# Kernel optimization log

Hardware: AMD Instinct MI355X
Metric: run time of the kernel (lower is better)

## Reference

```python
import jax, jax.numpy as jnp
import numpy as np

C = 64            # in_channels
IC = C // 2       # inter_channels (channel_rate=2)
R = 16            # reduction_ratio
EPS = 1e-5


def setup_inputs() -> dict:
    key = jax.random.key(0)
    ks = jax.random.split(key, 16)
    s = 0.05
    return {
        "x": jax.random.normal(ks[0], (16, C, 64, 25), dtype=jnp.float32),
        # 1x1 conv projections (common_v, key, query): [out, in] + bias
        "Wv": jax.random.normal(ks[1], (IC, C), dtype=jnp.float32) * s,
        "bv": jax.random.normal(ks[2], (IC,), dtype=jnp.float32) * s,
        "Wk": jax.random.normal(ks[3], (IC, C), dtype=jnp.float32) * s,
        "bk": jax.random.normal(ks[4], (IC,), dtype=jnp.float32) * s,
        "Wq": jax.random.normal(ks[5], (IC, C), dtype=jnp.float32) * s,
        "bq": jax.random.normal(ks[6], (IC,), dtype=jnp.float32) * s,
        # Trans_s: conv1x1 back to C + BatchNorm2d params (nonzero so output is non-trivial)
        "Wt": jax.random.normal(ks[7], (C, IC), dtype=jnp.float32) * s,
        "bt": jax.random.normal(ks[8], (C,), dtype=jnp.float32) * s,
        "gamma": jax.random.normal(ks[9], (C,), dtype=jnp.float32) * 0.5 + 1.0,
        "beta": jax.random.normal(ks[10], (C,), dtype=jnp.float32) * s,
        # ChannelGate MLP: Linear(C, C//R), Linear(C//R, C)
        "W1": jax.random.normal(ks[11], (C // R, C), dtype=jnp.float32) * s,
        "b1": jax.random.normal(ks[12], (C // R,), dtype=jnp.float32) * s,
        "W2": jax.random.normal(ks[13], (C, C // R), dtype=jnp.float32) * s,
        "b2": jax.random.normal(ks[14], (C,), dtype=jnp.float32) * s,
    }


def _conv1x1(x, W, b):
    # x: [N, Cin, T, V]; W: [Cout, Cin]
    return jnp.einsum('nctv,oc->notv', x, W) + b[None, :, None, None]


def reference(x, Wv, bv, Wk, bk, Wq, bq, Wt, bt, gamma, beta, W1, b1, W2, b2):
    N, Cc, T, V = x.shape
    TV = T * V
    ic = Wv.shape[0]

    v_x = _conv1x1(x, Wv, bv).reshape(N, ic, TV).transpose(0, 2, 1)  # [N, TV, ic]
    k_x = _conv1x1(x, Wk, bk).reshape(N, ic, TV).transpose(0, 2, 1)  # [N, TV, ic]
    q_x = _conv1x1(x, Wq, bq).reshape(N, ic, TV)                      # [N, ic, TV]

    # Unscaled dot-product attention over TV tokens (full [N, TV, TV] matrix)
    A = jnp.einsum('nti,nis->nts', k_x, q_x)
    attn = jax.nn.softmax(A, axis=-1)
    p = jnp.einsum('nts,nsi->nti', attn, v_x)                         # [N, TV, ic]
    p = p.transpose(0, 2, 1).reshape(N, ic, T, V)

    # Trans_s: conv1x1 + BatchNorm2d (training-mode batch statistics)
    p = _conv1x1(p, Wt, bt)
    mean = p.mean(axis=(0, 2, 3), keepdims=True)
    var = p.var(axis=(0, 2, 3), keepdims=True)
    p = (p - mean) * jax.lax.rsqrt(var + EPS)
    p = p * gamma[None, :, None, None] + beta[None, :, None, None]

    # ChannelGate (avg pool only) applied to original x
    avg = x.mean(axis=(2, 3))                                          # [N, C]
    h = jax.nn.relu(avg @ W1.T + b1)
    gate = jax.nn.sigmoid(h @ W2.T + b2)                               # [N, C]

    return gate[:, :, None, None] * p + x
```

## Files before the change

kernel.cpp:

```cpp
#include <hip/hip_runtime.h>
#include <hip/hip_bf16.h>
#include <math.h>

#define NB   16
#define CC   64
#define ICH  32
#define TV   1600
#define NTV  (NB*TV)

typedef __bf16 bf16x8 __attribute__((ext_vector_type(8)));
typedef __bf16 bf16x4 __attribute__((ext_vector_type(4)));
typedef float  f32x4  __attribute__((ext_vector_type(4)));

__global__ __launch_bounds__(256) void proj_gate_kernel(
    const float* __restrict__ x,
    const float* __restrict__ Wv, const float* __restrict__ bv,
    const float* __restrict__ Wk, const float* __restrict__ bk,
    const float* __restrict__ Wq, const float* __restrict__ bq,
    __bf16* __restrict__ Qb, __bf16* __restrict__ Kb,
    __bf16* __restrict__ VTb, float* __restrict__ AVG) {
  if (blockIdx.x >= 1248) {
    int b = blockIdx.x - 1248;
    int n = b >> 2, cq = b & 3;
    int c16 = threadIdx.x >> 4, l = threadIdx.x & 15;
    int c = cq * 16 + c16;
    const float4* xp = (const float4*)(x + ((size_t)n * CC + c) * TV) + l;
    float s = 0.f;
#pragma unroll
    for (int i = 0; i < 25; ++i) {
      float4 v = xp[i * 16];
      s += v.x + v.y + v.z + v.w;
    }
#pragma unroll
    for (int off = 8; off >= 1; off >>= 1) s += __shfl_down(s, off, 16);
    if (l == 0) AVG[n * CC + c] = s * (1.0f / (float)TV);
    return;
  }

  int r = blockIdx.x & 7;
  int i = blockIdx.x >> 3;
  int g = i / 12, sub = i % 12;
  int tile = r + 8 * g;
  if (tile >= 100) return;

  int p = sub >> 2, og = sub & 3;
  int ob = og * 8;
  int tvIdx = tile * 256 + threadIdx.x;
  int n = tvIdx / TV, tv = tvIdx % TV;

  const float* W; const float* B;
  if (p == 0)      { W = Wv; B = bv; }
  else if (p == 1) { W = Wk; B = bk; }
  else             { W = Wq; B = bq; }

  float acc[8];
#pragma unroll
  for (int j = 0; j < 8; ++j) acc[j] = B[ob + j];

  const float* xp = x + (size_t)n * CC * TV + tv;
#pragma unroll 16
  for (int c = 0; c < CC; ++c) {
    float xc = xp[c * TV];
#pragma unroll
    for (int j = 0; j < 8; ++j)
      acc[j] = fmaf(W[(ob + j) * CC + c], xc, acc[j]);
  }

  if (p == 0) {
#pragma unroll
    for (int j = 0; j < 8; ++j)
      VTb[(n * ICH + ob + j) * TV + tv] = (__bf16)acc[j];
  } else {
    if (p == 1) {
#pragma unroll
      for (int j = 0; j < 8; ++j)
        acc[j] *= 1.4426950408889634f;
    }
    bf16x8 t;
#pragma unroll
    for (int j = 0; j < 8; ++j) t[j] = (__bf16)acc[j];
    int base = (n * TV + tv) * ICH + ob;
    if (p == 1) *(bf16x8*)(Qb + base) = t;
    else        *(bf16x8*)(Kb + base) = t;
  }
}

__global__ __launch_bounds__(256) void attn_kernel(
    const __bf16* __restrict__ Qb, const __bf16* __restrict__ Kb,
    const __bf16* __restrict__ VTb, __bf16* __restrict__ P,
    const float* __restrict__ Wt, const float* __restrict__ bt,
    float* __restrict__ GSP) {
  __shared__ float smem_f[7936];
  int b = blockIdx.x;
  int r8 = b & 7, qq = b >> 3;
  int n = r8 * 2 + (qq >= 50 ? 1 : 0);
  int rowTile = (qq >= 50) ? qq - 50 : qq;
  int row0 = rowTile * 32;

  int w = threadIdx.x >> 6;
  int lane = threadIdx.x & 63;
  int m = lane & 15, q = lane >> 4;

  __bf16* Pw = (__bf16*)smem_f + w * 2304;

  const __bf16* Qn = Qb  + (size_t)n * TV * ICH;
  const __bf16* Kn = Kb  + (size_t)n * TV * ICH;
  const __bf16* Vn = VTb + (size_t)n * ICH * TV;

  bf16x8 aQ0 = *(const bf16x8*)(Qn + (row0 + m) * ICH + q * 8);
  bf16x8 aQ1 = *(const bf16x8*)(Qn + (row0 + 16 + m) * ICH + q * 8);

  f32x4 o00 = {0.f,0.f,0.f,0.f}, o01 = {0.f,0.f,0.f,0.f};
  f32x4 o10 = {0.f,0.f,0.f,0.f}, o11 = {0.f,0.f,0.f,0.f};
  float ls0 = 0.f, ls1 = 0.f;
  const f32x4 zero = {0.f,0.f,0.f,0.f};

  int ow = (w + b) & 3;
  int nch = (ow == 0) ? 7 : 6;

  bf16x8 bKc[4];
  {
    int s0 = ow * 64;
#pragma unroll
    for (int st = 0; st < 4; ++st)
      bKc[st] = *(const bf16x8*)(Kn + (s0 + st * 16 + m) * ICH + q * 8);
  }

  for (int j = 0; j < nch; ++j) {
    int s0 = (4 * j + ow) * 64;
#pragma unroll
    for (int st = 0; st < 4; ++st) {
      f32x4 a0 = __builtin_amdgcn_mfma_f32_16x16x32_bf16(bKc[st], aQ0, zero, 0, 0, 0);
      f32x4 a1 = __builtin_amdgcn_mfma_f32_16x16x32_bf16(bKc[st], aQ1, zero, 0, 0, 0);
      bf16x4 t0, t1;
#pragma unroll
      for (int r = 0; r < 4; ++r) {
        float e0 = __builtin_amdgcn_exp2f(a0[r]); ls0 += e0; t0[r] = (__bf16)e0;
        float e1 = __builtin_amdgcn_exp2f(a1[r]); ls1 += e1; t1[r] = (__bf16)e1;
      }
      int off = m * 72 + st * 16 + q * 4;
      *(bf16x4*)(Pw + off)        = t0;
      *(bf16x4*)(Pw + 1152 + off) = t1;
    }
    int chn = 4 * (j + 1) + ow;
    int s0n = (chn < 25 ? chn : 0) * 64;
    bf16x8 bKn[4], pV[2][2];
#pragma unroll
    for (int st = 0; st < 4; ++st)
      bKn[st] = *(const bf16x8*)(Kn + (s0n + st * 16 + m) * ICH + q * 8);
#pragma unroll
    for (int kc = 0; kc < 2; ++kc)
#pragma unroll
      for (int ict = 0; ict < 2; ++ict)
        pV[kc][ict] = *(const bf16x8*)(Vn + (ict * 16 + m) * TV + s0 + kc * 32 + q * 8);
    asm volatile("s_waitcnt lgkmcnt(0)" ::: "memory");
#pragma unroll
    for (int kc = 0; kc < 2; ++kc) {
      bf16x8 aP0 = *(const bf16x8*)(Pw + m * 72 + kc * 32 + q * 8);
      bf16x8 aP1 = *(const bf16x8*)(Pw + 1152 + m * 72 + kc * 32 + q * 8);
      o00 = __builtin_amdgcn_mfma_f32_16x16x32_bf16(aP0, pV[kc][0], o00, 0, 0, 0);
      o10 = __builtin_amdgcn_mfma_f32_16x16x32_bf16(aP1, pV[kc][0], o10, 0, 0, 0);
      o01 = __builtin_amdgcn_mfma_f32_16x16x32_bf16(aP0, pV[kc][1], o01, 0, 0, 0);
      o11 = __builtin_amdgcn_mfma_f32_16x16x32_bf16(aP1, pV[kc][1], o11, 0, 0, 0);
    }
#pragma unroll
    for (int st = 0; st < 4; ++st) bKc[st] = bKn[st];
  }

  ls0 += __shfl_xor(ls0, 16, 64); ls0 += __shfl_xor(ls0, 32, 64);
  ls1 += __shfl_xor(ls1, 16, 64); ls1 += __shfl_xor(ls1, 32, 64);
  f32x4 lv0, lv1;
#pragma unroll
  for (int r = 0; r < 4; ++r) {
    int src = q * 4 + r;
    lv0[r] = __shfl(ls0, src, 64);
    lv1[r] = __shfl(ls1, src, 64);
  }

  float* pub = smem_f;
  float* Pl  = smem_f + 6144;
  float* red = smem_f + 7296;

  __syncthreads();
  f32x4* mp = (f32x4*)(pub + (w * 64 + lane) * 24);
  mp[0] = o00; mp[1] = o01; mp[2] = o10; mp[3] = o11;
  mp[4] = lv0; mp[5] = lv1;
  __syncthreads();

  {
    int lsIdx = 4 + (w >> 1);
    const f32x4* p0 = (const f32x4*)(pub + lane * 24);
    f32x4 osum = p0[w];
    f32x4 lsum = p0[lsIdx];
#pragma unroll
    for (int ww = 1; ww < 4; ++ww) {
      const f32x4* pp = (const f32x4*)(pub + (ww * 64 + lane) * 24);
      f32x4 ov = pp[w], lv = pp[lsIdx];
#pragma unroll
      for (int r = 0; r < 4; ++r) { osum[r] += ov[r]; lsum[r] += lv[r]; }
    }
    int tile = w >> 1, colh = (w & 1) * 16;
#pragma unroll
    for (int r = 0; r < 4; ++r) {
      float p = osum[r] / lsum[r];
      int row = tile * 16 + q * 4 + r;
      P[(n * TV + row0 + row) * ICH + colh + m] = (__bf16)p;
      Pl[row * 36 + colh + m] = p;
    }
  }
  __syncthreads();

  int c = threadIdx.x & 63;
  float wr[ICH];
#pragma unroll
  for (int i = 0; i < ICH; ++i) wr[i] = Wt[c * ICH + i];
  float bc = bt[c];
  float sy = 0.f, sy2 = 0.f;
#pragma unroll
  for (int rr = 0; rr < 8; ++rr) {
    const f32x4* pr = (const f32x4*)(Pl + (w * 8 + rr) * 36);
    float y = bc;
#pragma unroll
    for (int u = 0; u < 8; ++u) {
      f32x4 pv = pr[u];
#pragma unroll
      for (int k = 0; k < 4; ++k) y = fmaf(wr[u * 4 + k], pv[k], y);
    }
    sy += y; sy2 += y * y;
  }
  red[w * 128 + c]      = sy;
  red[w * 128 + 64 + c] = sy2;
  __syncthreads();
  if (threadIdx.x < 128) {
    int t = threadIdx.x;
    float s = red[t] + red[128 + t] + red[256 + t] + red[384 + t];
    GSP[(size_t)t * 800 + blockIdx.x] = s;
  }
}

__global__ __launch_bounds__(256) void apply_kernel(
    const __bf16* __restrict__ P, const float* __restrict__ Wt,
    const float* __restrict__ bt, const float* __restrict__ GSP,
    const float* __restrict__ gamma, const float* __restrict__ beta,
    const float* __restrict__ AVG,
    const float* __restrict__ W1, const float* __restrict__ b1,
    const float* __restrict__ W2, const float* __restrict__ b2,
    const float* __restrict__ x, float* __restrict__ out) {
  int r = blockIdx.x & 7;
  int i = blockIdx.x >> 3;
  int cg = i & 7, h = i >> 3;
  int tb = r + 8 * h;
  if (tb >= 100) return;

  int tvIdx = tb * 256 + threadIdx.x;
  int n = tvIdx / TV, tv = tvIdx % TV;

  __shared__ float sstat[16];
  __shared__ float sSS[16];
  __shared__ float sG[8];

  {
    int colid = threadIdx.x >> 4;
    int sub = threadIdx.x & 15;
    int c8 = colid & 7;
    int gc = (colid < 8) ? (cg * 8 + c8) : (64 + cg * 8 + c8);
    const float* gp = GSP + (size_t)gc * 800;
    float s = 0.f;
#pragma unroll
    for (int k = 0; k < 50; ++k) s += gp[sub + k * 16];
#pragma unroll
    for (int off = 8; off >= 1; off >>= 1) s += __shfl_down(s, off, 16);
    if (sub == 0) sstat[colid] = s;
  }
  __syncthreads();
  if (threadIdx.x < 8) {
    int c8 = threadIdx.x;
    int c = cg * 8 + c8;
    float mean = sstat[c8] * (1.f / (float)NTV);
    float var  = sstat[8 + c8] * (1.f / (float)NTV) - mean * mean;
    float scale = rsqrtf(var + 1e-5f) * gamma[c];
    sSS[c8] = scale;
    sSS[8 + c8] = beta[c] - mean * scale;
    float hh[4];
#pragma unroll
    for (int jj = 0; jj < 4; ++jj) {
      float hv = b1[jj];
      for (int c2 = 0; c2 < CC; ++c2)
        hv = fmaf(W1[jj * CC + c2], AVG[n * CC + c2], hv);
      hh[jj] = fmaxf(hv, 0.f);
    }
    float g = b2[c];
#pragma unroll
    for (int jj = 0; jj < 4; ++jj) g = fmaf(W2[c * 4 + jj], hh[jj], g);
    sG[c8] = 1.f / (1.f + __expf(-g));
  }
  __syncthreads();

  float f[ICH];
  const bf16x8* pp = (const bf16x8*)(P + ((size_t)(n * TV + tv)) * ICH);
#pragma unroll
  for (int u = 0; u < 4; ++u) {
    bf16x8 v = pp[u];
#pragma unroll
    for (int j = 0; j < 8; ++j) f[u * 8 + j] = (float)v[j];
  }

#pragma unroll
  for (int j = 0; j < 8; ++j) {
    int c = cg * 8 + j;
    float y = bt[c];
#pragma unroll
    for (int ii = 0; ii < ICH; ++ii) y = fmaf(Wt[c * ICH + ii], f[ii], y);
    size_t idx = ((size_t)(n * CC + c)) * TV + tv;
    out[idx] = sG[j] * fmaf(y, sSS[j], sSS[8 + j]) + x[idx];
  }
}

extern "C" void kernel_launch(void* const* d_in, const int* in_sizes, int n_in,
                              void* d_out, int out_size, void* d_ws, size_t ws_size,
                              hipStream_t stream) {
  const float* x     = (const float*)d_in[0];
  const float* Wv    = (const float*)d_in[1];
  const float* bv    = (const float*)d_in[2];
  const float* Wk    = (const float*)d_in[3];
  const float* bk    = (const float*)d_in[4];
  const float* Wq    = (const float*)d_in[5];
  const float* bq    = (const float*)d_in[6];
  const float* Wt    = (const float*)d_in[7];
  const float* bt    = (const float*)d_in[8];
  const float* gamma = (const float*)d_in[9];
  const float* beta  = (const float*)d_in[10];
  const float* W1    = (const float*)d_in[11];
  const float* b1    = (const float*)d_in[12];
  const float* W2    = (const float*)d_in[13];
  const float* b2    = (const float*)d_in[14];
  float* out = (float*)d_out;
  char* ws = (char*)d_ws;

  const size_t E = 819200;
  __bf16* Qb  = (__bf16*)(ws);
  __bf16* Kb  = (__bf16*)(ws + 2*E);
  __bf16* VTb = (__bf16*)(ws + 4*E);
  __bf16* Pb  = (__bf16*)(ws + 6*E);
  float*  GSP = (float*) (ws + 8*E);
  float*  AVG = (float*) (ws + 8*E + 409600);

  proj_gate_kernel<<<1312, 256, 0, stream>>>(x, Wv, bv, Wk, bk, Wq, bq,
                                             Qb, Kb, VTb, AVG);
  attn_kernel<<<NB * 50, 256, 0, stream>>>(Qb, Kb, VTb, Pb, Wt, bt, GSP);
  apply_kernel<<<832, 256, 0, stream>>>(Pb, Wt, bt, GSP, gamma, beta, AVG,
                                        W1, b1, W2, b2, x, out);
}
```

Measured before the change: 134.7 us.

## Store Trans_s conv output from attention kernel and prefetch V one chunk ahead

Measured after the change: 139.1 us. 3.3% more time.

```diff
diff --git a/kernel.cpp b/kernel.cpp
--- a/kernel.cpp
+++ b/kernel.cpp
@@ -87,7 +87,7 @@
 
 __global__ __launch_bounds__(256) void attn_kernel(
     const __bf16* __restrict__ Qb, const __bf16* __restrict__ Kb,
-    const __bf16* __restrict__ VTb, __bf16* __restrict__ P,
+    const __bf16* __restrict__ VTb, float* __restrict__ Yb,
     const float* __restrict__ Wt, const float* __restrict__ bt,
     float* __restrict__ GSP) {
   __shared__ float smem_f[7936];
@@ -118,16 +118,22 @@
   int ow = (w + b) & 3;
   int nch = (ow == 0) ? 7 : 6;
 
-  bf16x8 bKc[4];
+  bf16x8 bKc[4], pVc[2][2];
   {
     int s0 = ow * 64;
 #pragma unroll
     for (int st = 0; st < 4; ++st)
       bKc[st] = *(const bf16x8*)(Kn + (s0 + st * 16 + m) * ICH + q * 8);
+#pragma unroll
+    for (int kc = 0; kc < 2; ++kc)
+#pragma unroll
+      for (int ict = 0; ict < 2; ++ict)
+        pVc[kc][ict] = *(const bf16x8*)(Vn + (ict * 16 + m) * TV + s0 + kc * 32 + q * 8);
   }
 
   for (int j = 0; j < nch; ++j) {
     int s0 = (4 * j + ow) * 64;
+    (void)s0;
 #pragma unroll
     for (int st = 0; st < 4; ++st) {
       f32x4 a0 = __builtin_amdgcn_mfma_f32_16x16x32_bf16(bKc[st], aQ0, zero, 0, 0, 0);
@@ -144,7 +150,7 @@
     }
     int chn = 4 * (j + 1) + ow;
     int s0n = (chn < 25 ? chn : 0) * 64;
-    bf16x8 bKn[4], pV[2][2];
+    bf16x8 bKn[4], pVn[2][2];
 #pragma unroll
     for (int st = 0; st < 4; ++st)
       bKn[st] = *(const bf16x8*)(Kn + (s0n + st * 16 + m) * ICH + q * 8);
@@ -152,19 +158,23 @@
     for (int kc = 0; kc < 2; ++kc)
 #pragma unroll
       for (int ict = 0; ict < 2; ++ict)
-        pV[kc][ict] = *(const bf16x8*)(Vn + (ict * 16 + m) * TV + s0 + kc * 32 + q * 8);
+        pVn[kc][ict] = *(const bf16x8*)(Vn + (ict * 16 + m) * TV + s0n + kc * 32 + q * 8);
     asm volatile("s_waitcnt lgkmcnt(0)" ::: "memory");
 #pragma unroll
     for (int kc = 0; kc < 2; ++kc) {
       bf16x8 aP0 = *(const bf16x8*)(Pw + m * 72 + kc * 32 + q * 8);
       bf16x8 aP1 = *(const bf16x8*)(Pw + 1152 + m * 72 + kc * 32 + q * 8);
-      o00 = __builtin_amdgcn_mfma_f32_16x16x32_bf16(aP0, pV[kc][0], o00, 0, 0, 0);
-      o10 = __builtin_amdgcn_mfma_f32_16x16x32_bf16(aP1, pV[kc][0], o10, 0, 0, 0);
-      o01 = __builtin_amdgcn_mfma_f32_16x16x32_bf16(aP0, pV[kc][1], o01, 0, 0, 0);
-      o11 = __builtin_amdgcn_mfma_f32_16x16x32_bf16(aP1, pV[kc][1], o11, 0, 0, 0);
+      o00 = __builtin_amdgcn_mfma_f32_16x16x32_bf16(aP0, pVc[kc][0], o00, 0, 0, 0);
+      o10 = __builtin_amdgcn_mfma_f32_16x16x32_bf16(aP1, pVc[kc][0], o10, 0, 0, 0);
+      o01 = __builtin_amdgcn_mfma_f32_16x16x32_bf16(aP0, pVc[kc][1], o01, 0, 0, 0);
+      o11 = __builtin_amdgcn_mfma_f32_16x16x32_bf16(aP1, pVc[kc][1], o11, 0, 0, 0);
     }
 #pragma unroll
     for (int st = 0; st < 4; ++st) bKc[st] = bKn[st];
+#pragma unroll
+    for (int kc = 0; kc < 2; ++kc)
+#pragma unroll
+      for (int ict = 0; ict < 2; ++ict) pVc[kc][ict] = pVn[kc][ict];
   }
 
   ls0 += __shfl_xor(ls0, 16, 64); ls0 += __shfl_xor(ls0, 32, 64);
@@ -204,7 +214,6 @@
     for (int r = 0; r < 4; ++r) {
       float p = osum[r] / lsum[r];
       int row = tile * 16 + q * 4 + r;
-      P[(n * TV + row0 + row) * ICH + colh + m] = (__bf16)p;
       Pl[row * 36 + colh + m] = p;
     }
   }
@@ -216,6 +225,7 @@
   for (int i = 0; i < ICH; ++i) wr[i] = Wt[c * ICH + i];
   float bc = bt[c];
   float sy = 0.f, sy2 = 0.f;
+  float* yout = Yb + (size_t)c * NTV + n * TV + row0 + w * 8;
 #pragma unroll
   for (int rr = 0; rr < 8; ++rr) {
     const f32x4* pr = (const f32x4*)(Pl + (w * 8 + rr) * 36);
@@ -226,6 +236,7 @@
 #pragma unroll
       for (int k = 0; k < 4; ++k) y = fmaf(wr[u * 4 + k], pv[k], y);
     }
+    yout[rr] = y;
     sy += y; sy2 += y * y;
   }
   red[w * 128 + c]      = sy;
@@ -234,13 +245,12 @@
   if (threadIdx.x < 128) {
     int t = threadIdx.x;
     float s = red[t] + red[128 + t] + red[256 + t] + red[384 + t];
-    GSP[(size_t)t * 800 + blockIdx.x] = s;
+    GSP[(size_t)t * 800 + b] = s;
   }
 }
 
 __global__ __launch_bounds__(256) void apply_kernel(
-    const __bf16* __restrict__ P, const float* __restrict__ Wt,
-    const float* __restrict__ bt, const float* __restrict__ GSP,
+    const float* __restrict__ Yb, const float* __restrict__ GSP,
     const float* __restrict__ gamma, const float* __restrict__ beta,
     const float* __restrict__ AVG,
     const float* __restrict__ W1, const float* __restrict__ b1,
@@ -296,21 +306,10 @@
   }
   __syncthreads();
 
-  float f[ICH];
-  const bf16x8* pp = (const bf16x8*)(P + ((size_t)(n * TV + tv)) * ICH);
-#pragma unroll
-  for (int u = 0; u < 4; ++u) {
-    bf16x8 v = pp[u];
-#pragma unroll
-    for (int j = 0; j < 8; ++j) f[u * 8 + j] = (float)v[j];
-  }
-
 #pragma unroll
   for (int j = 0; j < 8; ++j) {
     int c = cg * 8 + j;
-    float y = bt[c];
-#pragma unroll
-    for (int ii = 0; ii < ICH; ++ii) y = fmaf(Wt[c * ICH + ii], f[ii], y);
+    float y = Yb[(size_t)c * NTV + n * TV + tv];
     size_t idx = ((size_t)(n * CC + c)) * TV + tv;
     out[idx] = sG[j] * fmaf(y, sSS[j], sSS[8 + j]) + x[idx];
   }
@@ -341,13 +340,13 @@
   __bf16* Qb  = (__bf16*)(ws);
   __bf16* Kb  = (__bf16*)(ws + 2*E);
   __bf16* VTb = (__bf16*)(ws + 4*E);
-  __bf16* Pb  = (__bf16*)(ws + 6*E);
-  float*  GSP = (float*) (ws + 8*E);
-  float*  AVG = (float*) (ws + 8*E + 409600);
+  float*  Yb  = (float*) (ws + 6*E);
+  float*  GSP = (float*) (ws + 6*E + 6553600);
+  float*  AVG = (float*) (ws + 6*E + 6553600 + 409600);
 
   proj_gate_kernel<<<1312, 256, 0, stream>>>(x, Wv, bv, Wk, bk, Wq, bq,
                                              Qb, Kb, VTb, AVG);
-  attn_kernel<<<NB * 50, 256, 0, stream>>>(Qb, Kb, VTb, Pb, Wt, bt, GSP);
-  apply_kernel<<<832, 256, 0, stream>>>(Pb, Wt, bt, GSP, gamma, beta, AVG,
+  attn_kernel<<<NB * 50, 256, 0, stream>>>(Qb, Kb, VTb, Yb, Wt, bt, GSP);
+  apply_kernel<<<832, 256, 0, stream>>>(Yb, GSP, gamma, beta, AVG,
                                         W1, b1, W2, b2, x, out);
 }
```
